# Kernel tuning notes

Hardware: AMD Instinct MI355X
Metric: run time of the kernel (lower is better)

Reference implementation:

```python
import jax, jax.numpy as jnp
import numpy as np

NUM_EMBEDDINGS = 512
EMBEDDING_DIM = 64
COMMITMENT_COST = 0.25
N = 262144


def setup_inputs() -> dict:
    key = jax.random.key(0)
    k1, k2 = jax.random.split(key)
    inputs = jax.random.normal(k1, (N, EMBEDDING_DIM), dtype=jnp.float32)
    # torch init: uniform(-1/num_embeddings, 1/num_embeddings)
    emb_weight = jax.random.uniform(
        k2, (NUM_EMBEDDINGS, EMBEDDING_DIM), dtype=jnp.float32,
        minval=-1.0 / NUM_EMBEDDINGS, maxval=1.0 / NUM_EMBEDDINGS)
    return {"inputs": inputs, "emb_weight": emb_weight}


def reference(inputs, emb_weight):
    # squared L2 distances to every codebook entry: [N, K]
    distances = (jnp.sum(inputs ** 2, axis=1, keepdims=True)
                 + jnp.sum(emb_weight ** 2, axis=1)
                 - 2.0 * inputs @ emb_weight.T)
    encoding_indices = jnp.argmin(distances, axis=1)          # [N]
    quantized = emb_weight[encoding_indices]                  # direct gather == onehot @ W

    e_latent_loss = jnp.mean((jax.lax.stop_gradient(quantized) - inputs) ** 2)
    q_latent_loss = jnp.mean((quantized - jax.lax.stop_gradient(inputs)) ** 2)
    loss = q_latent_loss + COMMITMENT_COST * e_latent_loss

    # straight-through estimator
    quantized_st = inputs + jax.lax.stop_gradient(quantized - inputs)

    # avg_probs = mean over rows of the one-hot encodings -> normalized histogram
    counts = jnp.zeros((NUM_EMBEDDINGS,), dtype=jnp.float32).at[encoding_indices].add(1.0)
    avg_probs = counts / inputs.shape[0]
    perplexity = jnp.exp(-jnp.sum(avg_probs * jnp.log(avg_probs + 1e-10)))
    norm_perplexity = perplexity / NUM_EMBEDDINGS

    return (loss, quantized_st, norm_perplexity, encoding_indices[:, None])
```

## Files before the change

### kernel.cpp

```cpp
#include <hip/hip_runtime.h>

#define N_ROWS 262144
#define DIM 64
#define KCODES 512
#define THREADS 512
#define BLK_ROWS 256
#define NBLOCKS (N_ROWS / BLK_ROWS)
#define CHUNK 128
#define NCHUNK (KCODES / CHUNK)
#define NPART 64
#define MARGIN_T 1.25e-4f

#define OFF_Q 1
#define OFF_PERP (1 + (size_t)N_ROWS * DIM)
#define OFF_IDX (2 + (size_t)N_ROWS * DIM)

typedef __attribute__((ext_vector_type(8))) short bf16x8;
typedef __attribute__((ext_vector_type(4))) float f32x4;


__device__ __forceinline__ float np_sum_sq64(const float* __restrict__ v) {
#pragma clang fp contract(off)
    float r[8];
#pragma unroll
    for (int l = 0; l < 8; ++l) r[l] = v[l] * v[l];
#pragma unroll
    for (int k = 1; k < 8; ++k) {
#pragma unroll
        for (int l = 0; l < 8; ++l) {
            float sq = v[8 * k + l] * v[8 * k + l];
            r[l] = r[l] + sq;
        }
    }
    return ((r[0] + r[1]) + (r[2] + r[3])) + ((r[4] + r[5]) + (r[6] + r[7]));
}

__device__ __forceinline__ unsigned short f2bf(float f) {
    unsigned u = __float_as_uint(f);
    u += 0x7FFFu + ((u >> 16) & 1u);
    return (unsigned short)(u >> 16);
}
__device__ __forceinline__ float bf2f(unsigned short h) {
    return __uint_as_float((unsigned)h << 16);
}

__device__ __forceinline__ unsigned t2key_biased(float tb, unsigned idx) {
    return (__float_as_uint(tb) & 0xFFFFFE00u) | idx;
}
__device__ __forceinline__ float key2t(unsigned key) {
    return __uint_as_float(key & 0xFFFFFE00u) - 0.5f;
}


__global__ __launch_bounds__(256) void vq_prep(const float* __restrict__ W,
        unsigned short* __restrict__ WhiG, unsigned short* __restrict__ WloG,
        float* __restrict__ Bsc) {
    int c = blockIdx.x * 256 + threadIdx.x;
    if (c >= KCODES) return;
    const float* w = W + (size_t)c * DIM;
    Bsc[c] = np_sum_sq64(w);
#pragma unroll 4
    for (int d = 0; d < DIM; ++d) {
        float v = -2.0f * w[d];
        unsigned short hi = f2bf(v);
        unsigned short lo = f2bf(v - bf2f(hi));
        WhiG[c * DIM + d] = hi;
        WloG[c * DIM + d] = lo;
    }
}


__global__ __launch_bounds__(THREADS, 4) void vq_argmin(
    const float* __restrict__ X,
    const unsigned short* __restrict__ WhiG,
    const unsigned short* __restrict__ WloG,
    const float* __restrict__ Bsc,
    float* __restrict__ out,
    double* __restrict__ sseAcc,
    unsigned* __restrict__ gHistP,
    int* __restrict__ flagList,
    unsigned* __restrict__ gCnt) {

    __shared__ __align__(16) unsigned short sHi[CHUNK * DIM];
    __shared__ __align__(16) unsigned short sLo[CHUNK * DIM];
    __shared__ __align__(16) float sB[KCODES];
    __shared__ unsigned sHist[KCODES];
    __shared__ int sFlagRows[BLK_ROWS];
    __shared__ unsigned sCnt, sBase;
    __shared__ double sSseW[8];

    const int tid = threadIdx.x;
    const int w = tid >> 6;
    const int l = tid & 63;
    const int q = l >> 4;
    const int r16 = l & 15;
    const int R0 = blockIdx.x * BLK_ROWS;

    sB[tid] = Bsc[tid] + 0.5f;
    sHist[tid] = 0u;
    if (tid == 0) sCnt = 0u;

    bf16x8 xhA[2], xlA[2], xhB[2], xlB[2];
    float asumA = 0.f, asumB = 0.f;
    {
        const float* xrA = X + (size_t)(R0 + w * 32 + r16) * DIM;
        const float* xrB = xrA + 16 * DIM;
#pragma unroll
        for (int h = 0; h < 2; ++h) {
            float4 fa = *(const float4*)(xrA + 32 * h + 8 * q);
            float4 fb = *(const float4*)(xrA + 32 * h + 8 * q + 4);
            float fA[8] = {fa.x, fa.y, fa.z, fa.w, fb.x, fb.y, fb.z, fb.w};
            float4 ga = *(const float4*)(xrB + 32 * h + 8 * q);
            float4 gb = *(const float4*)(xrB + 32 * h + 8 * q + 4);
            float fB[8] = {ga.x, ga.y, ga.z, ga.w, gb.x, gb.y, gb.z, gb.w};
            bf16x8 hiA, loA, hiB, loB;
#pragma unroll
            for (int j = 0; j < 8; ++j) {
                asumA = fmaf(fA[j], fA[j], asumA);
                unsigned short h1 = f2bf(fA[j]);
                hiA[j] = (short)h1; loA[j] = (short)f2bf(fA[j] - bf2f(h1));
                asumB = fmaf(fB[j], fB[j], asumB);
                unsigned short h2 = f2bf(fB[j]);
                hiB[j] = (short)h2; loB[j] = (short)f2bf(fB[j] - bf2f(h2));
            }
            xhA[h] = hiA; xlA[h] = loA;
            xhB[h] = hiB; xlB[h] = loB;
        }
    }

    unsigned min1A = 0xFFFFFFFFu, min2A = 0xFFFFFFFFu;
    unsigned min1B = 0xFFFFFFFFu, min2B = 0xFFFFFFFFu;

    for (int cc = 0; cc < NCHUNK; ++cc) {
        const int c0 = cc * CHUNK;
        __syncthreads();
        {
            const uint4* gh = (const uint4*)(WhiG + (size_t)c0 * DIM);
            const uint4* gl = (const uint4*)(WloG + (size_t)c0 * DIM);
            char* bh = (char*)sHi; char* bl = (char*)sLo;
#pragma unroll
            for (int i = 0; i < (CHUNK * DIM / 8) / THREADS; ++i) {
                int idx = tid + THREADS * i;
                int c = idx >> 3, k8 = idx & 7;
                int off = (c * 128 + k8 * 16) ^ ((c & 7) << 4);
                *(uint4*)(bh + off) = gh[idx];
                *(uint4*)(bl + off) = gl[idx];
            }
        }
        __syncthreads();

#pragma unroll
        for (int ct = 0; ct < CHUNK / 16; ++ct) {
            const int cloc = ct * 16 + r16;
            const char* bh = (const char*)sHi;
            const char* bl = (const char*)sLo;
            const int sw = (cloc & 7) << 4;
            int o0 = (cloc * 128 + 16 * q) ^ sw;
            int o1 = (cloc * 128 + 64 + 16 * q) ^ sw;
            bf16x8 ah0 = *(const bf16x8*)(bh + o0);
            bf16x8 ah1 = *(const bf16x8*)(bh + o1);
            bf16x8 al0 = *(const bf16x8*)(bl + o0);
            bf16x8 al1 = *(const bf16x8*)(bl + o1);

            f32x4 accA = *(const f32x4*)&sB[c0 + ct * 16 + q * 4];
            f32x4 accB = accA;

            accA = __builtin_amdgcn_mfma_f32_16x16x32_bf16(ah0, xhA[0], accA, 0, 0, 0);
            accB = __builtin_amdgcn_mfma_f32_16x16x32_bf16(ah0, xhB[0], accB, 0, 0, 0);
            accA = __builtin_amdgcn_mfma_f32_16x16x32_bf16(ah1, xhA[1], accA, 0, 0, 0);
            accB = __builtin_amdgcn_mfma_f32_16x16x32_bf16(ah1, xhB[1], accB, 0, 0, 0);
            accA = __builtin_amdgcn_mfma_f32_16x16x32_bf16(ah0, xlA[0], accA, 0, 0, 0);
            accB = __builtin_amdgcn_mfma_f32_16x16x32_bf16(ah0, xlB[0], accB, 0, 0, 0);
            accA = __builtin_amdgcn_mfma_f32_16x16x32_bf16(ah1, xlA[1], accA, 0, 0, 0);
            accB = __builtin_amdgcn_mfma_f32_16x16x32_bf16(ah1, xlB[1], accB, 0, 0, 0);
            accA = __builtin_amdgcn_mfma_f32_16x16x32_bf16(al0, xhA[0], accA, 0, 0, 0);
            accB = __builtin_amdgcn_mfma_f32_16x16x32_bf16(al0, xhB[0], accB, 0, 0, 0);
            accA = __builtin_amdgcn_mfma_f32_16x16x32_bf16(al1, xhA[1], accA, 0, 0, 0);
            accB = __builtin_amdgcn_mfma_f32_16x16x32_bf16(al1, xhB[1], accB, 0, 0, 0);

            const unsigned jbase = (unsigned)(c0 + ct * 16 + q * 4);
            {
                unsigned k0 = t2key_biased(accA[0], jbase + 0u);
                unsigned k1 = t2key_biased(accA[1], jbase + 1u);
                unsigned k2 = t2key_biased(accA[2], jbase + 2u);
                unsigned k3 = t2key_biased(accA[3], jbase + 3u);
                unsigned lo01 = k0 < k1 ? k0 : k1, hi01 = k0 < k1 ? k1 : k0;
                unsigned lo23 = k2 < k3 ? k2 : k3, hi23 = k2 < k3 ? k3 : k2;
                unsigned m1 = lo01 < lo23 ? lo01 : lo23;
                unsigned mm = lo01 < lo23 ? lo23 : lo01;
                unsigned hh = hi01 < hi23 ? hi01 : hi23;
                unsigned m2 = hh < mm ? hh : mm;
                unsigned nm = min1A < m1 ? m1 : min1A;
                min1A = min1A < m1 ? min1A : m1;
                unsigned sm = min2A < m2 ? min2A : m2;
                min2A = sm < nm ? sm : nm;
            }
            {
                unsigned k0 = t2key_biased(accB[0], jbase + 0u);
                unsigned k1 = t2key_biased(accB[1], jbase + 1u);
                unsigned k2 = t2key_biased(accB[2], jbase + 2u);
                unsigned k3 = t2key_biased(accB[3], jbase + 3u);
                unsigned lo01 = k0 < k1 ? k0 : k1, hi01 = k0 < k1 ? k1 : k0;
                unsigned lo23 = k2 < k3 ? k2 : k3, hi23 = k2 < k3 ? k3 : k2;
                unsigned m1 = lo01 < lo23 ? lo01 : lo23;
                unsigned mm = lo01 < lo23 ? lo23 : lo01;
                unsigned hh = hi01 < hi23 ? hi01 : hi23;
                unsigned m2 = hh < mm ? hh : mm;
                unsigned nm = min1B < m1 ? m1 : min1B;
                min1B = min1B < m1 ? min1B : m1;
                unsigned sm = min2B < m2 ? min2B : m2;
                min2B = sm < nm ? sm : nm;
            }
        }
    }

#pragma unroll
    for (int d = 16; d <= 32; d <<= 1) {
        unsigned o1 = (unsigned)__shfl_xor((int)min1A, d, 64);
        unsigned o2 = (unsigned)__shfl_xor((int)min2A, d, 64);
        asumA += __shfl_xor(asumA, d, 64);
        unsigned n1 = min1A < o1 ? min1A : o1;
        unsigned mx = min1A > o1 ? min1A : o1;
        unsigned mn = min2A < o2 ? min2A : o2;
        min2A = mn < mx ? mn : mx; min1A = n1;

        unsigned p1 = (unsigned)__shfl_xor((int)min1B, d, 64);
        unsigned p2 = (unsigned)__shfl_xor((int)min2B, d, 64);
        asumB += __shfl_xor(asumB, d, 64);
        unsigned m1 = min1B < p1 ? min1B : p1;
        unsigned my = min1B > p1 ? min1B : p1;
        unsigned mz = min2B < p2 ? min2B : p2;
        min2B = mz < my ? mz : my; min1B = m1;
    }

    float ssev = 0.f;
    if (q == 0) {
        const int rowA = R0 + w * 32 + r16;
        const int rowB = rowA + 16;
        const unsigned bestA = min1A & 511u;
        const unsigned bestB = min1B & 511u;
        const float t1A = key2t(min1A), t2A = key2t(min2A);
        const float t1B = key2t(min1B), t2B = key2t(min2B);
        const bool flagA = (t2A < t1A + MARGIN_T);
        const bool flagB = (t2B < t1B + MARGIN_T);
        out[OFF_IDX + rowA] = (float)bestA;
        out[OFF_IDX + rowB] = (float)bestB;
        if (!flagA) { ssev += asumA + t1A; atomicAdd(&sHist[bestA], 1u); }
        else { unsigned s = atomicAdd(&sCnt, 1u); sFlagRows[s] = rowA; }
        if (!flagB) { ssev += asumB + t1B; atomicAdd(&sHist[bestB], 1u); }
        else { unsigned s = atomicAdd(&sCnt, 1u); sFlagRows[s] = rowB; }
    }
#pragma unroll
    for (int off = 32; off; off >>= 1) ssev += __shfl_down(ssev, off);
    if (l == 0) sSseW[w] = (double)ssev;
    __syncthreads();

    if (tid == 0) sBase = atomicAdd(gCnt, sCnt);
    {
        unsigned c = sHist[tid];
        if (c) atomicAdd(&gHistP[(blockIdx.x & (NPART - 1)) * KCODES + tid], c);
    }
    __syncthreads();
    if (tid < (int)sCnt) flagList[sBase + tid] = sFlagRows[tid];
    if (tid == 0) {
        double s = 0.0;
#pragma unroll
        for (int i = 0; i < 8; ++i) s += sSseW[i];
        atomicAdd(sseAcc, s);
    }
}


__global__ __launch_bounds__(512, 2) void vq_fixup(
    const float* __restrict__ X, const float* __restrict__ W,
    const float* __restrict__ Bsc, float* __restrict__ out,
    double* __restrict__ sseP, unsigned* __restrict__ gHistP,
    const int* __restrict__ flagList, const unsigned* __restrict__ gCnt) {
    __shared__ unsigned long long sKeyW[8];
    const unsigned total = *gCnt;
    const int t = threadIdx.x;
    const int wv = t >> 6, l = t & 63;

    for (unsigned i = blockIdx.x; i < total; i += gridDim.x) {
        const int row = flagList[i];

        float xr[DIM];
        {
            const float4* Xr4 = (const float4*)(X + (size_t)row * DIM);
#pragma unroll
            for (int k4 = 0; k4 < 16; ++k4) {
                float4 v = Xr4[k4];
                xr[4 * k4 + 0] = v.x; xr[4 * k4 + 1] = v.y;
                xr[4 * k4 + 2] = v.z; xr[4 * k4 + 3] = v.w;
            }
        }
        const float A = np_sum_sq64(xr);

        double acc = 0.0;
        {
            const float4* wr = (const float4*)(W + (size_t)t * DIM);
#pragma unroll
            for (int k4 = 0; k4 < 16; ++k4) {
                float4 f = wr[k4];
                acc = fma((double)f.x, (double)xr[4 * k4 + 0], acc);
                acc = fma((double)f.y, (double)xr[4 * k4 + 1], acc);
                acc = fma((double)f.z, (double)xr[4 * k4 + 2], acc);
                acc = fma((double)f.w, (double)xr[4 * k4 + 3], acc);
            }
        }
        unsigned long long bk;
        {
#pragma clang fp contract(off)
            float C2 = (float)(2.0 * acc);
            float e = (A + Bsc[t]) - C2;
            int iu = __float_as_int(e);
            unsigned u = ((unsigned)iu) ^ (((unsigned)(iu >> 31)) | 0x80000000u);
            bk = ((unsigned long long)u << 32) | (unsigned)t;
        }
#pragma unroll
        for (int d = 1; d < 64; d <<= 1) {
            unsigned long long o =
                (unsigned long long)__shfl_xor((long long)bk, d, 64);
            bk = bk < o ? bk : o;
        }
        if (l == 0) sKeyW[wv] = bk;
        __syncthreads();
        if (t == 0) {
            unsigned long long b = sKeyW[0];
#pragma unroll
            for (int k = 1; k < 8; ++k) if (sKeyW[k] < b) b = sKeyW[k];
            unsigned bestc = (unsigned)(b & 511ULL);
            unsigned u = (unsigned)(b >> 32);
            unsigned fb = (u & 0x80000000u) ? (u & 0x7FFFFFFFu) : ~u;
            float ebest = __uint_as_float(fb);
            out[OFF_IDX + row] = (float)bestc;
            atomicAdd(&gHistP[(i & (NPART - 1)) * KCODES + bestc], 1u);
            atomicAdd(&sseP[i & (NPART - 1)], (double)ebest);
        }
        __syncthreads();
    }
}


__global__ __launch_bounds__(256) void vq_scatter(
    const float* __restrict__ W, float* __restrict__ out) {
    const int gid = blockIdx.x * 256 + threadIdx.x;
    const int row = gid >> 6;
    const int lane = gid & 63;
    int idx = (int)out[OFF_IDX + row];
    if ((unsigned)idx >= KCODES) idx = KCODES - 1;
    out[OFF_Q + (size_t)row * DIM + lane] = W[(size_t)idx * DIM + lane];
}


__global__ __launch_bounds__(512) void vq_finalize(
    const double* __restrict__ sseAcc, const double* __restrict__ sseP,
    const unsigned* __restrict__ gHistP, float* __restrict__ out) {
    __shared__ float partial[8];
    const int t = threadIdx.x;
    unsigned c = 0;
#pragma unroll 8
    for (int p = 0; p < NPART; ++p) c += gHistP[p * KCODES + t];
    float pf = (float)c * (1.0f / (float)N_ROWS);
    float v = pf * logf(pf + 1e-10f);
#pragma unroll
    for (int off = 32; off; off >>= 1) v += __shfl_down(v, off);
    if ((t & 63) == 0) partial[t >> 6] = v;
    __syncthreads();
    if (t == 0) {
        float s = 0.f;
#pragma unroll
        for (int i = 0; i < 8; ++i) s += partial[i];
        out[OFF_PERP] = expf(-s) * (1.0f / (float)KCODES);
        double s2 = sseAcc[0];
#pragma unroll
        for (int i = 0; i < NPART; ++i) s2 += sseP[i];
        out[0] = (float)(1.25 * s2 * (1.0 / ((double)N_ROWS * (double)DIM)));
    }
}

extern "C" void kernel_launch(void* const* d_in, const int* in_sizes, int n_in,
                              void* d_out, int out_size, void* d_ws, size_t ws_size,
                              hipStream_t stream) {
    const float* X = (const float*)d_in[0];
    const float* W = (const float*)d_in[1];
    float* out = (float*)d_out;
    double* sseAcc = (double*)d_ws;
    double* sseP = (double*)((char*)d_ws + 64);
    unsigned* gCnt = (unsigned*)((char*)d_ws + 64 + NPART * sizeof(double));

    size_t zb = 64 + NPART * sizeof(double) + 64;
    if (zb > ws_size) zb = ws_size;
    hipMemsetAsync(d_ws, 0, zb, stream);

    uintptr_t sbase = ((uintptr_t)(out + OFF_Q) + 15) & ~(uintptr_t)15;
    unsigned short* WhiG = (unsigned short*)sbase;
    unsigned short* WloG = WhiG + (size_t)KCODES * DIM;
    float* Bsc = (float*)(WloG + (size_t)KCODES * DIM);
    unsigned* gHistP = (unsigned*)(Bsc + KCODES);
    int* flagList = (int*)(gHistP + (size_t)NPART * KCODES);
    hipMemsetAsync(gHistP, 0, (size_t)NPART * KCODES * sizeof(unsigned), stream);

    vq_prep<<<2, 256, 0, stream>>>(W, WhiG, WloG, Bsc);
    vq_argmin<<<NBLOCKS, THREADS, 0, stream>>>(X, WhiG, WloG, Bsc, out,
                                               sseAcc, gHistP, flagList, gCnt);
    vq_fixup<<<NBLOCKS, 512, 0, stream>>>(X, W, Bsc, out, sseP, gHistP,
                                          flagList, gCnt);
    vq_finalize<<<1, 512, 0, stream>>>(sseAcc, sseP, gHistP, out);
    vq_scatter<<<(N_ROWS * DIM) / 256, 256, 0, stream>>>(W, out);
}
```

Measured before the change: 241.8 us.

## Fold memsets into prep kernel, track float top-2, tighten margin, raise occupancy

Two memset calls are dropped and the workspace zeroing (histograms, SSE accumulators, counter) now happens inside the prep kernel, which is launched with 64 blocks. The argmin loop no longer keeps a packed second-best key; it keeps the packed best key plus float best and second-best distances. The ambiguity margin is reduced so fewer rows go to the exact fixup pass. Launch-bounds occupancy hints are raised for argmin and fixup, which caps registers and may cause spills, and the smaller margin risks wrong indices on near-ties.

```diff
diff --git a/kernel.cpp b/kernel.cpp
--- a/kernel.cpp
+++ b/kernel.cpp
@@ -9,7 +9,7 @@
 #define CHUNK 128
 #define NCHUNK (KCODES / CHUNK)
 #define NPART 64
-#define MARGIN_T 1.25e-4f
+#define MARGIN_T 4.0e-5f
 
 #define OFF_Q 1
 #define OFF_PERP (1 + (size_t)N_ROWS * DIM)
@@ -47,15 +47,21 @@
 __device__ __forceinline__ unsigned t2key_biased(float tb, unsigned idx) {
     return (__float_as_uint(tb) & 0xFFFFFE00u) | idx;
 }
-__device__ __forceinline__ float key2t(unsigned key) {
-    return __uint_as_float(key & 0xFFFFFE00u) - 0.5f;
-}
 
 
 __global__ __launch_bounds__(256) void vq_prep(const float* __restrict__ W,
         unsigned short* __restrict__ WhiG, unsigned short* __restrict__ WloG,
-        float* __restrict__ Bsc) {
-    int c = blockIdx.x * 256 + threadIdx.x;
+        float* __restrict__ Bsc, unsigned* __restrict__ gHistP,
+        double* __restrict__ sseAcc, double* __restrict__ sseP,
+        unsigned* __restrict__ gCnt) {
+    const int tid = threadIdx.x, b = blockIdx.x;
+    gHistP[b * KCODES + tid] = 0u;
+    gHistP[b * KCODES + tid + 256] = 0u;
+    if (b == 0) {
+        if (tid < NPART) sseP[tid] = 0.0;
+        if (tid == 0) { sseAcc[0] = 0.0; *gCnt = 0u; }
+    }
+    int c = b * 256 + tid;
     if (c >= KCODES) return;
     const float* w = W + (size_t)c * DIM;
     Bsc[c] = np_sum_sq64(w);
@@ -70,7 +76,7 @@
 }
 
 
-__global__ __launch_bounds__(THREADS, 4) void vq_argmin(
+__global__ __launch_bounds__(THREADS, 6) void vq_argmin(
     const float* __restrict__ X,
     const unsigned short* __restrict__ WhiG,
     const unsigned short* __restrict__ WloG,
@@ -128,8 +134,9 @@
         }
     }
 
-    unsigned min1A = 0xFFFFFFFFu, min2A = 0xFFFFFFFFu;
-    unsigned min1B = 0xFFFFFFFFu, min2B = 0xFFFFFFFFu;
+    unsigned min1A = 0xFFFFFFFFu, min1B = 0xFFFFFFFFu;
+    float t1A = 3.4e38f, t2A = 3.4e38f;
+    float t1B = 3.4e38f, t2B = 3.4e38f;
 
     for (int cc = 0; cc < NCHUNK; ++cc) {
         const int c0 = cc * CHUNK;
@@ -184,53 +191,55 @@
                 unsigned k1 = t2key_biased(accA[1], jbase + 1u);
                 unsigned k2 = t2key_biased(accA[2], jbase + 2u);
                 unsigned k3 = t2key_biased(accA[3], jbase + 3u);
-                unsigned lo01 = k0 < k1 ? k0 : k1, hi01 = k0 < k1 ? k1 : k0;
-                unsigned lo23 = k2 < k3 ? k2 : k3, hi23 = k2 < k3 ? k3 : k2;
-                unsigned m1 = lo01 < lo23 ? lo01 : lo23;
-                unsigned mm = lo01 < lo23 ? lo23 : lo01;
-                unsigned hh = hi01 < hi23 ? hi01 : hi23;
-                unsigned m2 = hh < mm ? hh : mm;
-                unsigned nm = min1A < m1 ? m1 : min1A;
-                min1A = min1A < m1 ? min1A : m1;
-                unsigned sm = min2A < m2 ? min2A : m2;
-                min2A = sm < nm ? sm : nm;
+                unsigned ka = k0 < k1 ? k0 : k1, kb = k2 < k3 ? k2 : k3;
+                ka = ka < kb ? ka : kb;
+                min1A = min1A < ka ? min1A : ka;
+                float lo01 = fminf(accA[0], accA[1]), hi01 = fmaxf(accA[0], accA[1]);
+                float lo23 = fminf(accA[2], accA[3]), hi23 = fmaxf(accA[2], accA[3]);
+                float m1 = fminf(lo01, lo23);
+                float m2 = fminf(fmaxf(lo01, lo23), fminf(hi01, hi23));
+                float nm = fmaxf(t1A, m1);
+                t1A = fminf(t1A, m1);
+                t2A = fminf(fminf(t2A, m2), nm);
             }
             {
                 unsigned k0 = t2key_biased(accB[0], jbase + 0u);
                 unsigned k1 = t2key_biased(accB[1], jbase + 1u);
                 unsigned k2 = t2key_biased(accB[2], jbase + 2u);
                 unsigned k3 = t2key_biased(accB[3], jbase + 3u);
-                unsigned lo01 = k0 < k1 ? k0 : k1, hi01 = k0 < k1 ? k1 : k0;
-                unsigned lo23 = k2 < k3 ? k2 : k3, hi23 = k2 < k3 ? k3 : k2;
-                unsigned m1 = lo01 < lo23 ? lo01 : lo23;
-                unsigned mm = lo01 < lo23 ? lo23 : lo01;
-                unsigned hh = hi01 < hi23 ? hi01 : hi23;
-                unsigned m2 = hh < mm ? hh : mm;
-                unsigned nm = min1B < m1 ? m1 : min1B;
-                min1B = min1B < m1 ? min1B : m1;
-                unsigned sm = min2B < m2 ? min2B : m2;
-                min2B = sm < nm ? sm : nm;
+                unsigned ka = k0 < k1 ? k0 : k1, kb = k2 < k3 ? k2 : k3;
+                ka = ka < kb ? ka : kb;
+                min1B = min1B < ka ? min1B : ka;
+                float lo01 = fminf(accB[0], accB[1]), hi01 = fmaxf(accB[0], accB[1]);
+                float lo23 = fminf(accB[2], accB[3]), hi23 = fmaxf(accB[2], accB[3]);
+                float m1 = fminf(lo01, lo23);
+                float m2 = fminf(fmaxf(lo01, lo23), fminf(hi01, hi23));
+                float nm = fmaxf(t1B, m1);
+                t1B = fminf(t1B, m1);
+                t2B = fminf(fminf(t2B, m2), nm);
             }
         }
     }
 
 #pragma unroll
     for (int d = 16; d <= 32; d <<= 1) {
-        unsigned o1 = (unsigned)__shfl_xor((int)min1A, d, 64);
-        unsigned o2 = (unsigned)__shfl_xor((int)min2A, d, 64);
+        unsigned oA = (unsigned)__shfl_xor((int)min1A, d, 64);
+        min1A = min1A < oA ? min1A : oA;
+        float p1 = __shfl_xor(t1A, d, 64);
+        float p2 = __shfl_xor(t2A, d, 64);
+        float nm = fmaxf(t1A, p1);
+        t1A = fminf(t1A, p1);
+        t2A = fminf(fminf(t2A, p2), nm);
         asumA += __shfl_xor(asumA, d, 64);
-        unsigned n1 = min1A < o1 ? min1A : o1;
-        unsigned mx = min1A > o1 ? min1A : o1;
-        unsigned mn = min2A < o2 ? min2A : o2;
-        min2A = mn < mx ? mn : mx; min1A = n1;
-
-        unsigned p1 = (unsigned)__shfl_xor((int)min1B, d, 64);
-        unsigned p2 = (unsigned)__shfl_xor((int)min2B, d, 64);
+
+        unsigned oB = (unsigned)__shfl_xor((int)min1B, d, 64);
+        min1B = min1B < oB ? min1B : oB;
+        float q1 = __shfl_xor(t1B, d, 64);
+        float q2 = __shfl_xor(t2B, d, 64);
+        float nb = fmaxf(t1B, q1);
+        t1B = fminf(t1B, q1);
+        t2B = fminf(fminf(t2B, q2), nb);
         asumB += __shfl_xor(asumB, d, 64);
-        unsigned m1 = min1B < p1 ? min1B : p1;
-        unsigned my = min1B > p1 ? min1B : p1;
-        unsigned mz = min2B < p2 ? min2B : p2;
-        min2B = mz < my ? mz : my; min1B = m1;
     }
 
     float ssev = 0.f;
@@ -239,15 +248,13 @@
         const int rowB = rowA + 16;
         const unsigned bestA = min1A & 511u;
         const unsigned bestB = min1B & 511u;
-        const float t1A = key2t(min1A), t2A = key2t(min2A);
-        const float t1B = key2t(min1B), t2B = key2t(min2B);
         const bool flagA = (t2A < t1A + MARGIN_T);
         const bool flagB = (t2B < t1B + MARGIN_T);
         out[OFF_IDX + rowA] = (float)bestA;
         out[OFF_IDX + rowB] = (float)bestB;
-        if (!flagA) { ssev += asumA + t1A; atomicAdd(&sHist[bestA], 1u); }
+        if (!flagA) { ssev += asumA + (t1A - 0.5f); atomicAdd(&sHist[bestA], 1u); }
         else { unsigned s = atomicAdd(&sCnt, 1u); sFlagRows[s] = rowA; }
-        if (!flagB) { ssev += asumB + t1B; atomicAdd(&sHist[bestB], 1u); }
+        if (!flagB) { ssev += asumB + (t1B - 0.5f); atomicAdd(&sHist[bestB], 1u); }
         else { unsigned s = atomicAdd(&sCnt, 1u); sFlagRows[s] = rowB; }
     }
 #pragma unroll
@@ -271,7 +278,7 @@
 }
 
 
-__global__ __launch_bounds__(512, 2) void vq_fixup(
+__global__ __launch_bounds__(512, 6) void vq_fixup(
     const float* __restrict__ X, const float* __restrict__ W,
     const float* __restrict__ Bsc, float* __restrict__ out,
     double* __restrict__ sseP, unsigned* __restrict__ gHistP,
@@ -389,19 +396,15 @@
     double* sseP = (double*)((char*)d_ws + 64);
     unsigned* gCnt = (unsigned*)((char*)d_ws + 64 + NPART * sizeof(double));
 
-    size_t zb = 64 + NPART * sizeof(double) + 64;
-    if (zb > ws_size) zb = ws_size;
-    hipMemsetAsync(d_ws, 0, zb, stream);
-
     uintptr_t sbase = ((uintptr_t)(out + OFF_Q) + 15) & ~(uintptr_t)15;
     unsigned short* WhiG = (unsigned short*)sbase;
     unsigned short* WloG = WhiG + (size_t)KCODES * DIM;
     float* Bsc = (float*)(WloG + (size_t)KCODES * DIM);
     unsigned* gHistP = (unsigned*)(Bsc + KCODES);
     int* flagList = (int*)(gHistP + (size_t)NPART * KCODES);
-    hipMemsetAsync(gHistP, 0, (size_t)NPART * KCODES * sizeof(unsigned), stream);
-
-    vq_prep<<<2, 256, 0, stream>>>(W, WhiG, WloG, Bsc);
+
+    vq_prep<<<NPART, 256, 0, stream>>>(W, WhiG, WloG, Bsc, gHistP,
+                                       sseAcc, sseP, gCnt);
     vq_argmin<<<NBLOCKS, THREADS, 0, stream>>>(X, WhiG, WloG, Bsc, out,
                                                sseAcc, gHistP, flagList, gCnt);
     vq_fixup<<<NBLOCKS, 512, 0, stream>>>(X, W, Bsc, out, sseP, gHistP,
```

After: 318.4 us. 1.32x slower.
